# Optimization experiments

Hardware: AMD Instinct MI355X
Metric: run time of the kernel (lower is better)

## Reference

```python
import jax, jax.numpy as jnp
import numpy as np

N = 50000    # n_nodes
E = 800000   # n_edges (avg degree 16)
F_IN = 64    # node_features
F_H = 64     # filters


def setup_inputs() -> dict:
    key = jax.random.key(0)
    ks = jax.random.split(key, 24)
    p = lambda k, s: jax.random.normal(k, s, dtype=jnp.float32) * 0.05
    inp = {
        "x": jax.random.normal(ks[0], (N, F_IN), dtype=jnp.float32),
        "edge_index": jax.random.randint(ks[1], (2, E), 0, N, dtype=jnp.int32),
        "edge_weight": jax.random.uniform(ks[2], (E,), dtype=jnp.float32),
    }
    # 6 ChebConvs (K=2): conv_x_z, conv_h_z, conv_x_r, conv_h_r, conv_x_h, conv_h_h
    for i, nm in enumerate(["xz", "hz", "xr", "hr", "xh", "hh"]):
        fin = F_IN if nm[0] == "x" else F_H
        inp[f"W_{nm}0"] = p(ks[3 + 3 * i], (fin, F_H))
        inp[f"W_{nm}1"] = p(ks[4 + 3 * i], (fin, F_H))
        inp[f"b_{nm}"] = p(ks[5 + 3 * i], (F_H,))
    inp["W_lin"] = p(ks[21], (F_H, F_IN))
    inp["b_lin"] = p(ks[22], (F_IN,))
    return inp


def _forward(x, edge_weight, edge_index,
             W_xz0, W_xz1, b_xz, W_hz0, W_hz1, b_hz,
             W_xr0, W_xr1, b_xr, W_hr0, W_hr1, b_hr,
             W_xh0, W_xh1, b_xh, W_hh0, W_hh1, b_hh,
             W_lin, b_lin):
    row, col = edge_index[0], edge_index[1]
    # ChebConv K=2, sym normalization, lambda_max=2: L_hat = -D^{-1/2} A D^{-1/2}
    # (self-loops removed first, as in PyG ChebConv)
    w = jnp.where(row == col, 0.0, edge_weight)
    deg = jax.ops.segment_sum(w, row, num_segments=N)
    deg_safe = jnp.where(deg > 0, deg, 1.0)
    dinv = jnp.where(deg > 0, jax.lax.rsqrt(deg_safe), 0.0)
    norm = -dinv[row] * w * dinv[col]  # [E]

    def conv(v, W0, W1, b):
        # Tx_0 = v ; Tx_1 = L_hat @ v via gather-scatter along edges
        tx1 = jax.ops.segment_sum(norm[:, None] * v[row], col, num_segments=N)
        return v @ W0 + tx1 @ W1 + b

    H = jnp.zeros((N, F_H), dtype=x.dtype)  # initial hidden state
    Z = jax.nn.sigmoid(conv(x, W_xz0, W_xz1, b_xz) + conv(H, W_hz0, W_hz1, b_hz))
    R = jax.nn.sigmoid(conv(x, W_xr0, W_xr1, b_xr) + conv(H, W_hr0, W_hr1, b_hr))
    Ht = jnp.tanh(conv(x, W_xh0, W_xh1, b_xh) + conv(H * R, W_hh0, W_hh1, b_hh))
    H = Z * H + (1.0 - Z) * Ht
    return jax.nn.relu(H) @ W_lin + b_lin


def reference(x, edge_index, edge_weight,
              W_xz0, W_xz1, b_xz, W_hz0, W_hz1, b_hz,
              W_xr0, W_xr1, b_xr, W_hr0, W_hr1, b_hr,
              W_xh0, W_xh1, b_xh, W_hh0, W_hh1, b_hh,
              W_lin, b_lin):
    return _forward(x, edge_weight, edge_index,
                    W_xz0, W_xz1, b_xz, W_hz0, W_hz1, b_hz,
                    W_xr0, W_xr1, b_xr, W_hr0, W_hr1, b_hr,
                    W_xh0, W_xh1, b_xh, W_hh0, W_hh1, b_hh,
                    W_lin, b_lin)
```

## Files before the change

### kernel.cpp

```cpp
#include <hip/hip_runtime.h>

#define N_NODES 50000
#define N_EDGES 800000
#define F 64
#define NPAD 50048
#define NBUCK 196
#define NBLK 256
#define EPB (N_EDGES / NBLK)
#define BN 128
#define AIDX32(k, n) ((k) * 132 + ((k) >> 3) * 4 + (n))

typedef float f32x4 __attribute__((ext_vector_type(4)));
typedef short bf16x8 __attribute__((ext_vector_type(8)));

__device__ inline unsigned short f2bf(float f) {
    unsigned u = __float_as_uint(f);
    u = (u + 0x7FFFu + ((u >> 16) & 1u)) >> 16;
    return (unsigned short)u;
}

__global__ __launch_bounds__(256) void prep_w(const float* __restrict__ Wxz0,
                                              const float* __restrict__ Wxz1,
                                              const float* __restrict__ Wxh0,
                                              const float* __restrict__ Wxh1,
                                              const float* __restrict__ Wlin,
                                              unsigned short* __restrict__ wzT,
                                              unsigned short* __restrict__ whT,
                                              unsigned short* __restrict__ wlT) {
    int gid = blockIdx.x * 256 + threadIdx.x;
    int m = gid >> 12, idx = gid & 4095;
    int k = idx >> 6, f = idx & 63;
    const float* src;
    unsigned short* dst;
    if (m == 0)      { src = Wxz0; dst = wzT; }
    else if (m == 1) { src = Wxz1; dst = wzT + 4096; }
    else if (m == 2) { src = Wxh0; dst = whT; }
    else if (m == 3) { src = Wxh1; dst = whT + 4096; }
    else             { src = Wlin; dst = wlT; }
    dst[f * 64 + k] = f2bf(src[idx]);
}

__global__ __launch_bounds__(256) void prep_x(const float* __restrict__ x,
                                              unsigned short* __restrict__ xb) {
    int idx4 = blockIdx.x * 256 + threadIdx.x;
    int n = idx4 >> 4;
    ushort4 o = make_ushort4(0, 0, 0, 0);
    if (n < N_NODES) {
        float4 v = *(const float4*)&x[idx4 * 4];
        o = make_ushort4(f2bf(v.x), f2bf(v.y), f2bf(v.z), f2bf(v.w));
    }
    *(ushort4*)&xb[idx4 * 4] = o;
}

__global__ __launch_bounds__(256) void count_kernel(const int* __restrict__ ei,
                                                    int* __restrict__ cntC,
                                                    int* __restrict__ cntR) {
    __shared__ int histC[NBUCK], histR[NBUCK];
    const int t = threadIdx.x, blk = blockIdx.x;
    for (int i = t; i < NBUCK; i += 256) { histC[i] = 0; histR[i] = 0; }
    __syncthreads();
    const int e0 = blk * EPB;
    for (int i = t; i < EPB; i += 256) {
        int e = e0 + i;
        int r = ei[e], c = ei[N_EDGES + e];
        if (r != c) {
            atomicAdd(&histC[c >> 8], 1);
            atomicAdd(&histR[r >> 8], 1);
        }
    }
    __syncthreads();
    for (int i = t; i < NBUCK; i += 256) {
        cntC[i * NBLK + blk] = histC[i];
        cntR[i * NBLK + blk] = histR[i];
    }
}

__global__ __launch_bounds__(256) void scan1_kernel(int* __restrict__ cntC,
                                                    int* __restrict__ cntR,
                                                    int* __restrict__ btC,
                                                    int* __restrict__ btR) {
    __shared__ int wsum[4];
    const int t = threadIdx.x, g = blockIdx.x;
    int* cnt = (g < NBUCK) ? cntC : cntR;
    int* bt  = (g < NBUCK) ? btC : btR;
    const int bucket = (g < NBUCK) ? g : g - NBUCK;
    const int lane = t & 63, wid = t >> 6;
    int v = cnt[bucket * NBLK + t];
    int s = v;
#pragma unroll
    for (int d = 1; d < 64; d <<= 1) {
        int u = __shfl_up(s, d);
        if (lane >= d) s += u;
    }
    if (lane == 63) wsum[wid] = s;
    __syncthreads();
    int wbase = 0;
    for (int w = 0; w < wid; ++w) wbase += wsum[w];
    cnt[bucket * NBLK + t] = wbase + s - v;
    if (t == 255) bt[bucket] = wbase + s;
}

__global__ __launch_bounds__(256) void scan2_kernel(const int* __restrict__ btC,
                                                    const int* __restrict__ btR,
                                                    int* __restrict__ bbC,
                                                    int* __restrict__ bbR,
                                                    int* __restrict__ offs) {
    __shared__ int wsum[4];
    const int t = threadIdx.x;
    const int lane = t & 63, wid = t >> 6;
    {
        int v = (t < NBUCK) ? btC[t] : 0;
        int s = v;
#pragma unroll
        for (int d = 1; d < 64; d <<= 1) {
            int u = __shfl_up(s, d);
            if (lane >= d) s += u;
        }
        if (lane == 63) wsum[wid] = s;
        __syncthreads();
        int wbase = 0;
        for (int w = 0; w < wid; ++w) wbase += wsum[w];
        if (t < NBUCK) bbC[t] = wbase + s - v;
        if (t == 255) { bbC[NBUCK] = wbase + s; offs[N_NODES] = wbase + s; }
        __syncthreads();
    }
    {
        int v = (t < NBUCK) ? btR[t] : 0;
        int s = v;
#pragma unroll
        for (int d = 1; d < 64; d <<= 1) {
            int u = __shfl_up(s, d);
            if (lane >= d) s += u;
        }
        if (lane == 63) wsum[wid] = s;
        __syncthreads();
        int wbase = 0;
        for (int w = 0; w < wid; ++w) wbase += wsum[w];
        if (t < NBUCK) bbR[t] = wbase + s - v;
        if (t == 255) bbR[NBUCK] = wbase + s;
    }
}

__global__ __launch_bounds__(256) void place_kernel(const int* __restrict__ ei,
                                                    const float* __restrict__ ew,
                                                    const int* __restrict__ cntC,
                                                    const int* __restrict__ cntR,
                                                    const int* __restrict__ bbC,
                                                    const int* __restrict__ bbR,
                                                    uint2* __restrict__ colPart,
                                                    uint2* __restrict__ rowPart) {
    __shared__ int cursC[NBUCK], cursR[NBUCK];
    const int t = threadIdx.x, blk = blockIdx.x;
    for (int i = t; i < NBUCK; i += 256) {
        cursC[i] = bbC[i] + cntC[i * NBLK + blk];
        cursR[i] = bbR[i] + cntR[i * NBLK + blk];
    }
    __syncthreads();
    const int e0 = blk * EPB;
    for (int i = t; i < EPB; i += 256) {
        int e = e0 + i;
        int r = ei[e], c = ei[N_EDGES + e];
        if (r == c) continue;
        unsigned wbits = __float_as_uint(ew[e]);
        int pC = atomicAdd(&cursC[c >> 8], 1);
        colPart[pC] = make_uint2((unsigned)r | ((unsigned)(c & 255) << 16), wbits);
        int pR = atomicAdd(&cursR[r >> 8], 1);
        rowPart[pR] = make_uint2((unsigned)(r & 255), wbits);
    }
}

__global__ __launch_bounds__(256) void rowB_kernel(const uint2* __restrict__ rowPart,
                                                   const int* __restrict__ bbR,
                                                   float* __restrict__ dinv) {
    __shared__ float degL[256];
    const int t = threadIdx.x, b = blockIdx.x;
    degL[t] = 0.0f;
    __syncthreads();
    const int start = bbR[b], end = bbR[b + 1];
    for (int i = start + t; i < end; i += 256) {
        uint2 v = rowPart[i];
        atomicAdd(&degL[v.x], __uint_as_float(v.y));
    }
    __syncthreads();
    int n = b * 256 + t;
    if (n < N_NODES) {
        float d = degL[t];
        dinv[n] = (d > 0.0f) ? rsqrtf(d) : 0.0f;
    }
}

__global__ __launch_bounds__(256) void colB_kernel(const uint2* __restrict__ colPart,
                                                   const int* __restrict__ bbC,
                                                   const float* __restrict__ dinv,
                                                   int* __restrict__ offs,
                                                   uint2* __restrict__ edgesOut) {
    __shared__ int cntL[256];
    __shared__ int curL[256];
    __shared__ int wsum[4];
    const int t = threadIdx.x, b = blockIdx.x;
    const int lane = t & 63, wid = t >> 6;
    const int start = bbC[b], end = bbC[b + 1];
    cntL[t] = 0;
    __syncthreads();
    for (int i = start + t; i < end; i += 256) {
        uint2 v = colPart[i];
        atomicAdd(&cntL[(v.x >> 16) & 255], 1);
    }
    __syncthreads();
    int v = cntL[t];
    int s = v;
#pragma unroll
    for (int d = 1; d < 64; d <<= 1) {
        int u = __shfl_up(s, d);
        if (lane >= d) s += u;
    }
    if (lane == 63) wsum[wid] = s;
    __syncthreads();
    int wbase = 0;
    for (int w = 0; w < wid; ++w) wbase += wsum[w];
    int excl = wbase + s - v;
    curL[t] = excl;
    int n = b * 256 + t;
    if (n < N_NODES) offs[n] = start + excl;
    __syncthreads();
    for (int i = start + t; i < end; i += 256) {
        uint2 e = colPart[i];
        int cl = (e.x >> 16) & 255;
        int p = atomicAdd(&curL[cl], 1);
        int r = e.x & 0xFFFF;
        float wd = __uint_as_float(e.y) * dinv[r];
        edgesOut[start + p] = make_uint2((unsigned)r, __float_as_uint(wd));
    }
}

__global__ __launch_bounds__(256) void gather_kernel(const int* __restrict__ offs,
                                                     const uint2* __restrict__ edgesOut,
                                                     const float* __restrict__ dinv,
                                                     const float* __restrict__ x,
                                                     unsigned short* __restrict__ Sb) {
    int n = blockIdx.x * 4 + (threadIdx.x >> 6);
    int lane = threadIdx.x & 63;
    if (n >= N_NODES) return;
    int p = offs[n], end = offs[n + 1];
    float acc = 0.0f;
    for (int base = p; base < end; base += 32) {
        int rem = end - base;
        int sl = lane & 31;
        uint2 ev = make_uint2(0u, 0u);
        if (sl < rem) ev = edgesOut[base + sl];
        int myr = (int)ev.x;
        float mwd = __uint_as_float(ev.y);
        int cnt = min(rem, 32);
        int i = 0;
        for (; i + 4 <= cnt; i += 4) {
            int r0 = __shfl(myr, i + 0), r1 = __shfl(myr, i + 1);
            int r2 = __shfl(myr, i + 2), r3 = __shfl(myr, i + 3);
            float w0 = __shfl(mwd, i + 0), w1 = __shfl(mwd, i + 1);
            float w2 = __shfl(mwd, i + 2), w3 = __shfl(mwd, i + 3);
            float v0 = x[r0 * F + lane];
            float v1 = x[r1 * F + lane];
            float v2 = x[r2 * F + lane];
            float v3 = x[r3 * F + lane];
            acc = fmaf(w0, v0, acc);
            acc = fmaf(w1, v1, acc);
            acc = fmaf(w2, v2, acc);
            acc = fmaf(w3, v3, acc);
        }
        for (; i < cnt; ++i) {
            int r = __shfl(myr, i);
            float wd = __shfl(mwd, i);
            acc = fmaf(wd, x[r * F + lane], acc);
        }
    }
    Sb[n * F + lane] = f2bf(-dinv[n] * acc);
}

__global__ __launch_bounds__(256) void fused_mfma(
    const unsigned short* __restrict__ xb, const unsigned short* __restrict__ Sb,
    const unsigned short* __restrict__ wzT, const unsigned short* __restrict__ whT,
    const unsigned short* __restrict__ wlT,
    const float* __restrict__ bxz, const float* __restrict__ bhz,
    const float* __restrict__ bxh, const float* __restrict__ bhh,
    const float* __restrict__ blin, float* __restrict__ out) {
    __shared__ __align__(16) unsigned short Rlds[4 * 16 * 72];

    const int t = threadIdx.x;
    const int l = t & 63, wid = t >> 6;
    const int row16 = l & 15, quad = l >> 4;
    const int gn0 = blockIdx.x * 64 + wid * 16;

    f32x4 zacc[4], hacc[4];
#pragma unroll
    for (int ft = 0; ft < 4; ++ft) {
        int f = ft * 16 + row16;
        float bz = bxz[f] + bhz[f];
        float bh = bxh[f] + bhh[f];
        zacc[ft] = (f32x4){bz, bz, bz, bz};
        hacc[ft] = (f32x4){bh, bh, bh, bh};
    }

#pragma unroll
    for (int half = 0; half < 2; ++half) {
        const unsigned short* Ab = half ? Sb : xb;
        const unsigned short* Wzp = wzT + half * 4096;
        const unsigned short* Whp = whT + half * 4096;
#pragma unroll
        for (int ks = 0; ks < 2; ++ks) {
            bf16x8 a = *(const bf16x8*)(Ab + (size_t)(gn0 + row16) * 64 + ks * 32 + quad * 8);
#pragma unroll
            for (int ft = 0; ft < 4; ++ft) {
                bf16x8 bz8 = *(const bf16x8*)(Wzp + (ft * 16 + row16) * 64 + ks * 32 + quad * 8);
                bf16x8 bh8 = *(const bf16x8*)(Whp + (ft * 16 + row16) * 64 + ks * 32 + quad * 8);
                zacc[ft] = __builtin_amdgcn_mfma_f32_16x16x32_bf16(a, bz8, zacc[ft], 0, 0, 0);
                hacc[ft] = __builtin_amdgcn_mfma_f32_16x16x32_bf16(a, bh8, hacc[ft], 0, 0, 0);
            }
        }
    }

#pragma unroll
    for (int ft = 0; ft < 4; ++ft)
#pragma unroll
        for (int r = 0; r < 4; ++r) {
            float z = zacc[ft][r], h = hacc[ft][r];
            float zz = 1.0f / (1.0f + __expf(-z));
            float R = fmaxf((1.0f - zz) * tanhf(h), 0.0f);
            Rlds[wid * 1152 + (quad * 4 + r) * 72 + ft * 16 + row16] = f2bf(R);
        }

    f32x4 oacc[4];
#pragma unroll
    for (int ft = 0; ft < 4; ++ft) oacc[ft] = (f32x4){0.f, 0.f, 0.f, 0.f};
#pragma unroll
    for (int ks = 0; ks < 2; ++ks) {
        bf16x8 ra = *(const bf16x8*)&Rlds[wid * 1152 + row16 * 72 + ks * 32 + quad * 8];
#pragma unroll
        for (int ft = 0; ft < 4; ++ft) {
            bf16x8 wl8 = *(const bf16x8*)(wlT + (ft * 16 + row16) * 64 + ks * 32 + quad * 8);
            oacc[ft] = __builtin_amdgcn_mfma_f32_16x16x32_bf16(ra, wl8, oacc[ft], 0, 0, 0);
        }
    }
#pragma unroll
    for (int ft = 0; ft < 4; ++ft) {
        float bl = blin[ft * 16 + row16];
#pragma unroll
        for (int r = 0; r < 4; ++r) {
            int gn = gn0 + quad * 4 + r;
            if (gn < N_NODES) out[gn * 64 + ft * 16 + row16] = oacc[ft][r] + bl;
        }
    }
}

__global__ __launch_bounds__(256) void deg_fb(const int* __restrict__ ei,
                                              const float* __restrict__ ew,
                                              float* __restrict__ deg) {
    int e = blockIdx.x * blockDim.x + threadIdx.x;
    if (e >= N_EDGES) return;
    int r = ei[e];
    int c = ei[N_EDGES + e];
    if (r != c) atomicAdd(&deg[r], ew[e]);
}

__global__ __launch_bounds__(256) void dinv_kernel(const float* __restrict__ deg,
                                                   float* __restrict__ dinv) {
    int n = blockIdx.x * blockDim.x + threadIdx.x;
    if (n >= N_NODES) return;
    float d = deg[n];
    dinv[n] = (d > 0.0f) ? rsqrtf(d) : 0.0f;
}

__global__ __launch_bounds__(256) void scatter_fb(const int* __restrict__ ei,
                                                  const float* __restrict__ ew,
                                                  const float* __restrict__ x,
                                                  const float* __restrict__ dinv,
                                                  float* S) {
    int e = blockIdx.x * 4 + (threadIdx.x >> 6);
    int lane = threadIdx.x & 63;
    if (e >= N_EDGES) return;
    int r = ei[e];
    int c = ei[N_EDGES + e];
    if (r == c) return;
    float nrm = -dinv[r] * ew[e] * dinv[c];
    atomicAdd(&S[c * F + lane], nrm * x[r * F + lane]);
}

__global__ __launch_bounds__(128) void fused_fp32(
    const float* __restrict__ x, float* sOut,
    const float* __restrict__ Wxz0, const float* __restrict__ Wxz1,
    const float* __restrict__ Wxh0, const float* __restrict__ Wxh1,
    const float* __restrict__ bxz, const float* __restrict__ bhz,
    const float* __restrict__ bxh, const float* __restrict__ bhh,
    const float* __restrict__ Wlin, const float* __restrict__ blin) {
    __shared__ float P[8448];
    float* As = P;
    float* Wc = P + 4352;
    const int t = threadIdx.x;
    const int n0 = blockIdx.x * BN;
    const int ti = t >> 3;
    const int tj = t & 7;
    const int nb = ti * 8;
    const int f0 = tj * 8;

    float zacc[8][8], hacc[8][8];
#pragma unroll
    for (int j = 0; j < 8; ++j) {
        float bz = bxz[f0 + j] + bhz[f0 + j];
        float bh = bxh[f0 + j] + bhh[f0 + j];
#pragma unroll
        for (int i = 0; i < 8; ++i) { zacc[i][j] = bz; hacc[i][j] = bh; }
    }
    for (int half = 0; half < 2; ++half) {
        const float* Abase = half ? (const float*)sOut : x;
        const float* Wz = half ? Wxz1 : Wxz0;
        const float* Wh = half ? Wxh1 : Wxh0;
        for (int kc = 0; kc < 2; ++kc) {
            const int kb = kc * 32;
            __syncthreads();
#pragma unroll
            for (int rep = 0; rep < 8; ++rep) {
                int idx = rep * 128 + t;
                int nn = idx >> 3;
                int q = idx & 7;
                int gn = n0 + nn;
                float4 v = make_float4(0.f, 0.f, 0.f, 0.f);
                if (gn < N_NODES) v = *(const float4*)&Abase[gn * F + kb + q * 4];
                int k = q * 4;
                As[AIDX32(k + 0, nn)] = v.x;
                As[AIDX32(k + 1, nn)] = v.y;
                As[AIDX32(k + 2, nn)] = v.z;
                As[AIDX32(k + 3, nn)] = v.w;
            }
#pragma unroll
            for (int rep = 0; rep < 8; ++rep) {
                int idx = rep * 128 + t;
                int cq = idx & 31;
                int kk = idx >> 5;
                const float* src = (cq < 16) ? &Wz[(kb + kk) * F + cq * 4]
                                             : &Wh[(kb + kk) * F + (cq - 16) * 4];
                *(float4*)&Wc[kk * 128 + cq * 4] = *(const float4*)src;
            }
            __syncthreads();
#pragma unroll 8
            for (int kl = 0; kl < 32; ++kl) {
                const float* Ap = &As[AIDX32(kl, nb)];
                float4 a0 = *(const float4*)Ap;
                float4 a1 = *(const float4*)(Ap + 4);
                const float* Wp = &Wc[kl * 128 + f0];
                float4 wz0 = *(const float4*)Wp;
                float4 wz1 = *(const float4*)(Wp + 4);
                float4 wh0 = *(const float4*)(Wp + 64);
                float4 wh1 = *(const float4*)(Wp + 68);
                float a[8]  = {a0.x, a0.y, a0.z, a0.w, a1.x, a1.y, a1.z, a1.w};
                float wz[8] = {wz0.x, wz0.y, wz0.z, wz0.w, wz1.x, wz1.y, wz1.z, wz1.w};
                float wh[8] = {wh0.x, wh0.y, wh0.z, wh0.w, wh1.x, wh1.y, wh1.z, wh1.w};
#pragma unroll
                for (int i = 0; i < 8; ++i)
#pragma unroll
                    for (int j = 0; j < 8; ++j) {
                        zacc[i][j] = fmaf(a[i], wz[j], zacc[i][j]);
                        hacc[i][j] = fmaf(a[i], wh[j], hacc[i][j]);
                    }
            }
        }
    }
    __syncthreads();
#pragma unroll
    for (int j = 0; j < 8; ++j) {
        int f = f0 + j;
        float R[8];
#pragma unroll
        for (int i = 0; i < 8; ++i) {
            float zz = 1.0f / (1.0f + __expf(-zacc[i][j]));
            float hh = tanhf(hacc[i][j]);
            R[i] = fmaxf((1.0f - zz) * hh, 0.0f);
        }
        float* Rp = &P[f * 132 + nb];
        *(float4*)Rp = make_float4(R[0], R[1], R[2], R[3]);
        *(float4*)(Rp + 4) = make_float4(R[4], R[5], R[6], R[7]);
    }
    __syncthreads();
    float (*oacc)[8] = zacc;
#pragma unroll
    for (int j = 0; j < 8; ++j) {
        float bl = blin[f0 + j];
#pragma unroll
        for (int i = 0; i < 8; ++i) oacc[i][j] = bl;
    }
#pragma unroll 4
    for (int k = 0; k < 64; ++k) {
        const float* Rp = &P[k * 132 + nb];
        float4 a0 = *(const float4*)Rp;
        float4 a1 = *(const float4*)(Rp + 4);
        float4 w0 = *(const float4*)&Wlin[k * F + f0];
        float4 w1 = *(const float4*)&Wlin[k * F + f0 + 4];
        float a[8] = {a0.x, a0.y, a0.z, a0.w, a1.x, a1.y, a1.z, a1.w};
        float w[8] = {w0.x, w0.y, w0.z, w0.w, w1.x, w1.y, w1.z, w1.w};
#pragma unroll
        for (int i = 0; i < 8; ++i)
#pragma unroll
            for (int j = 0; j < 8; ++j)
                oacc[i][j] = fmaf(a[i], w[j], oacc[i][j]);
    }
#pragma unroll
    for (int i = 0; i < 8; ++i) {
        int gn = n0 + nb + i;
        if (gn < N_NODES) {
            *(float4*)&sOut[gn * F + f0] =
                make_float4(oacc[i][0], oacc[i][1], oacc[i][2], oacc[i][3]);
            *(float4*)&sOut[gn * F + f0 + 4] =
                make_float4(oacc[i][4], oacc[i][5], oacc[i][6], oacc[i][7]);
        }
    }
}

extern "C" void kernel_launch(void* const* d_in, const int* in_sizes, int n_in,
                              void* d_out, int out_size, void* d_ws, size_t ws_size,
                              hipStream_t stream) {
    const float* x    = (const float*)d_in[0];
    const int*   ei   = (const int*)d_in[1];
    const float* ew   = (const float*)d_in[2];
    const float* Wxz0 = (const float*)d_in[3];
    const float* Wxz1 = (const float*)d_in[4];
    const float* bxz  = (const float*)d_in[5];
    const float* bhz  = (const float*)d_in[8];
    const float* Wxh0 = (const float*)d_in[15];
    const float* Wxh1 = (const float*)d_in[16];
    const float* bxh  = (const float*)d_in[17];
    const float* bhh  = (const float*)d_in[20];
    const float* Wlin = (const float*)d_in[21];
    const float* blin = (const float*)d_in[22];
    float* outp = (float*)d_out;

    int*    cntC  = (int*)d_ws;
    int*    cntR  = cntC + NBUCK * NBLK;
    int*    btC   = cntR + NBUCK * NBLK;
    int*    btR   = btC + 256;
    int*    bbC   = btR + 256;
    int*    bbR   = bbC + 256;
    int*    offs  = bbR + 256;
    float*  dinv  = (float*)(offs + NPAD + 64);
    unsigned short* xb  = (unsigned short*)(dinv + NPAD);
    unsigned short* Sb  = xb + (size_t)NPAD * 64;
    unsigned short* wzT = Sb + (size_t)NPAD * 64;
    unsigned short* whT = wzT + 8192;
    unsigned short* wlT = whT + 8192;
    uint2*  colPart  = (uint2*)(wlT + 4096);
    uint2*  rowPart  = colPart + N_EDGES;
    uint2*  edgesOut = rowPart + N_EDGES;
    size_t needed = (size_t)(2 * NBUCK * NBLK + 1024 + NPAD + 64 + NPAD) * 4
                  + (size_t)NPAD * 64 * 2 * 2 + 40960
                  + (size_t)N_EDGES * 3 * 8 + 256;

    if (ws_size >= needed) {
        prep_w<<<80, 256, 0, stream>>>(Wxz0, Wxz1, Wxh0, Wxh1, Wlin, wzT, whT, wlT);
        prep_x<<<NPAD * 16 / 256, 256, 0, stream>>>(x, xb);
        count_kernel<<<NBLK, 256, 0, stream>>>(ei, cntC, cntR);
        scan1_kernel<<<2 * NBUCK, 256, 0, stream>>>(cntC, cntR, btC, btR);
        scan2_kernel<<<1, 256, 0, stream>>>(btC, btR, bbC, bbR, offs);
        place_kernel<<<NBLK, 256, 0, stream>>>(ei, ew, cntC, cntR, bbC, bbR,
                                               colPart, rowPart);
        rowB_kernel<<<NBUCK, 256, 0, stream>>>(rowPart, bbR, dinv);
        colB_kernel<<<NBUCK, 256, 0, stream>>>(colPart, bbC, dinv, offs, edgesOut);
        gather_kernel<<<(N_NODES + 3) / 4, 256, 0, stream>>>(offs, edgesOut, dinv,
                                                             x, Sb);
        fused_mfma<<<NPAD / 64, 256, 0, stream>>>(xb, Sb, wzT, whT, wlT,
                                                  bxz, bhz, bxh, bhh, blin, outp);
    } else {
        float* deg = (float*)d_ws;
        float* dv  = deg + NPAD;
        hipMemsetAsync(deg, 0, (size_t)NPAD * sizeof(float), stream);
        hipMemsetAsync(d_out, 0, (size_t)N_NODES * F * sizeof(float), stream);
        deg_fb<<<(N_EDGES + 255) / 256, 256, 0, stream>>>(ei, ew, deg);
        dinv_kernel<<<(N_NODES + 255) / 256, 256, 0, stream>>>(deg, dv);
        scatter_fb<<<N_EDGES / 4, 256, 0, stream>>>(ei, ew, x, dv, outp);
        fused_fp32<<<(N_NODES + BN - 1) / BN, 128, 0, stream>>>(
            x, outp, Wxz0, Wxz1, Wxh0, Wxh1, bxz, bhz, bxh, bhh, Wlin, blin);
    }
}
```

Baseline: 122.5 us.

## Replace CSR build plus gather with per-bucket LDS atomic accumulation

Column buckets shrink to 128 nodes, so each bucket's 128x64 fp32 partial sum fits in shared memory. A new 1024-thread kernel processes each bucket's edges directly, using shared-memory atomics instead of building a sorted per-node CSR (colB plus edgesOut) and running a separate gather pass. This removes one kernel launch and an 800k-edge intermediate write and read. The two prep kernels are also merged into one launch. The trade-off is LDS atomic contention, and fp32 summation order that is no longer deterministic.

```diff
diff --git a/kernel.cpp b/kernel.cpp
--- a/kernel.cpp
+++ b/kernel.cpp
@@ -4,7 +4,8 @@
 #define N_EDGES 800000
 #define F 64
 #define NPAD 50048
-#define NBUCK 196
+#define NBUCKC 392
+#define NBUCKR 196
 #define NBLK 256
 #define EPB (N_EDGES / NBLK)
 #define BN 128
@@ -19,60 +20,58 @@
     return (unsigned short)u;
 }
 
-__global__ __launch_bounds__(256) void prep_w(const float* __restrict__ Wxz0,
-                                              const float* __restrict__ Wxz1,
-                                              const float* __restrict__ Wxh0,
-                                              const float* __restrict__ Wxh1,
-                                              const float* __restrict__ Wlin,
-                                              unsigned short* __restrict__ wzT,
-                                              unsigned short* __restrict__ whT,
-                                              unsigned short* __restrict__ wlT) {
-    int gid = blockIdx.x * 256 + threadIdx.x;
-    int m = gid >> 12, idx = gid & 4095;
-    int k = idx >> 6, f = idx & 63;
-    const float* src;
-    unsigned short* dst;
-    if (m == 0)      { src = Wxz0; dst = wzT; }
-    else if (m == 1) { src = Wxz1; dst = wzT + 4096; }
-    else if (m == 2) { src = Wxh0; dst = whT; }
-    else if (m == 3) { src = Wxh1; dst = whT + 4096; }
-    else             { src = Wlin; dst = wlT; }
-    dst[f * 64 + k] = f2bf(src[idx]);
-}
-
-__global__ __launch_bounds__(256) void prep_x(const float* __restrict__ x,
-                                              unsigned short* __restrict__ xb) {
-    int idx4 = blockIdx.x * 256 + threadIdx.x;
-    int n = idx4 >> 4;
-    ushort4 o = make_ushort4(0, 0, 0, 0);
-    if (n < N_NODES) {
-        float4 v = *(const float4*)&x[idx4 * 4];
-        o = make_ushort4(f2bf(v.x), f2bf(v.y), f2bf(v.z), f2bf(v.w));
-    }
-    *(ushort4*)&xb[idx4 * 4] = o;
+__global__ __launch_bounds__(256) void prep_kernel(
+    const float* __restrict__ x,
+    const float* __restrict__ Wxz0, const float* __restrict__ Wxz1,
+    const float* __restrict__ Wxh0, const float* __restrict__ Wxh1,
+    const float* __restrict__ Wlin,
+    unsigned short* __restrict__ xb, unsigned short* __restrict__ wzT,
+    unsigned short* __restrict__ whT, unsigned short* __restrict__ wlT) {
+    int blk = blockIdx.x;
+    if (blk < 80) {
+        int gid = blk * 256 + threadIdx.x;
+        int m = gid >> 12, idx = gid & 4095;
+        int k = idx >> 6, f = idx & 63;
+        const float* src;
+        unsigned short* dst;
+        if (m == 0)      { src = Wxz0; dst = wzT; }
+        else if (m == 1) { src = Wxz1; dst = wzT + 4096; }
+        else if (m == 2) { src = Wxh0; dst = whT; }
+        else if (m == 3) { src = Wxh1; dst = whT + 4096; }
+        else             { src = Wlin; dst = wlT; }
+        dst[f * 64 + k] = f2bf(src[idx]);
+    } else {
+        int idx4 = (blk - 80) * 256 + threadIdx.x;
+        int n = idx4 >> 4;
+        ushort4 o = make_ushort4(0, 0, 0, 0);
+        if (n < N_NODES) {
+            float4 v = *(const float4*)&x[idx4 * 4];
+            o = make_ushort4(f2bf(v.x), f2bf(v.y), f2bf(v.z), f2bf(v.w));
+        }
+        *(ushort4*)&xb[idx4 * 4] = o;
+    }
 }
 
 __global__ __launch_bounds__(256) void count_kernel(const int* __restrict__ ei,
                                                     int* __restrict__ cntC,
                                                     int* __restrict__ cntR) {
-    __shared__ int histC[NBUCK], histR[NBUCK];
+    __shared__ int histC[NBUCKC], histR[NBUCKR];
     const int t = threadIdx.x, blk = blockIdx.x;
-    for (int i = t; i < NBUCK; i += 256) { histC[i] = 0; histR[i] = 0; }
+    for (int i = t; i < NBUCKC; i += 256) histC[i] = 0;
+    for (int i = t; i < NBUCKR; i += 256) histR[i] = 0;
     __syncthreads();
     const int e0 = blk * EPB;
     for (int i = t; i < EPB; i += 256) {
         int e = e0 + i;
         int r = ei[e], c = ei[N_EDGES + e];
         if (r != c) {
-            atomicAdd(&histC[c >> 8], 1);
+            atomicAdd(&histC[c >> 7], 1);
             atomicAdd(&histR[r >> 8], 1);
         }
     }
     __syncthreads();
-    for (int i = t; i < NBUCK; i += 256) {
-        cntC[i * NBLK + blk] = histC[i];
-        cntR[i * NBLK + blk] = histR[i];
-    }
+    for (int i = t; i < NBUCKC; i += 256) cntC[i * NBLK + blk] = histC[i];
+    for (int i = t; i < NBUCKR; i += 256) cntR[i * NBLK + blk] = histR[i];
 }
 
 __global__ __launch_bounds__(256) void scan1_kernel(int* __restrict__ cntC,
@@ -81,9 +80,9 @@
                                                     int* __restrict__ btR) {
     __shared__ int wsum[4];
     const int t = threadIdx.x, g = blockIdx.x;
-    int* cnt = (g < NBUCK) ? cntC : cntR;
-    int* bt  = (g < NBUCK) ? btC : btR;
-    const int bucket = (g < NBUCK) ? g : g - NBUCK;
+    int* cnt; int* bt; int bucket;
+    if (g < NBUCKC) { cnt = cntC; bt = btC; bucket = g; }
+    else            { cnt = cntR; bt = btR; bucket = g - NBUCKC; }
     const int lane = t & 63, wid = t >> 6;
     int v = cnt[bucket * NBLK + t];
     int s = v;
@@ -103,13 +102,14 @@
 __global__ __launch_bounds__(256) void scan2_kernel(const int* __restrict__ btC,
                                                     const int* __restrict__ btR,
                                                     int* __restrict__ bbC,
-                                                    int* __restrict__ bbR,
-                                                    int* __restrict__ offs) {
+                                                    int* __restrict__ bbR) {
     __shared__ int wsum[4];
     const int t = threadIdx.x;
     const int lane = t & 63, wid = t >> 6;
-    {
-        int v = (t < NBUCK) ? btC[t] : 0;
+    int total = 0;
+    for (int chunk = 0; chunk < 2; ++chunk) {
+        int i = chunk * 256 + t;
+        int v = (i < NBUCKC) ? btC[i] : 0;
         int s = v;
 #pragma unroll
         for (int d = 1; d < 64; d <<= 1) {
@@ -120,12 +120,14 @@
         __syncthreads();
         int wbase = 0;
         for (int w = 0; w < wid; ++w) wbase += wsum[w];
-        if (t < NBUCK) bbC[t] = wbase + s - v;
-        if (t == 255) { bbC[NBUCK] = wbase + s; offs[N_NODES] = wbase + s; }
+        if (i < NBUCKC) bbC[i] = total + wbase + s - v;
+        int btot = wsum[0] + wsum[1] + wsum[2] + wsum[3];
         __syncthreads();
-    }
+        total += btot;
+    }
+    if (t == 0) bbC[NBUCKC] = total;
     {
-        int v = (t < NBUCK) ? btR[t] : 0;
+        int v = (t < NBUCKR) ? btR[t] : 0;
         int s = v;
 #pragma unroll
         for (int d = 1; d < 64; d <<= 1) {
@@ -136,8 +138,8 @@
         __syncthreads();
         int wbase = 0;
         for (int w = 0; w < wid; ++w) wbase += wsum[w];
-        if (t < NBUCK) bbR[t] = wbase + s - v;
-        if (t == 255) bbR[NBUCK] = wbase + s;
+        if (t < NBUCKR) bbR[t] = wbase + s - v;
+        if (t == 255) bbR[NBUCKR] = wbase + s;
     }
 }
 
@@ -149,12 +151,10 @@
                                                     const int* __restrict__ bbR,
                                                     uint2* __restrict__ colPart,
                                                     uint2* __restrict__ rowPart) {
-    __shared__ int cursC[NBUCK], cursR[NBUCK];
+    __shared__ int cursC[NBUCKC], cursR[NBUCKR];
     const int t = threadIdx.x, blk = blockIdx.x;
-    for (int i = t; i < NBUCK; i += 256) {
-        cursC[i] = bbC[i] + cntC[i * NBLK + blk];
-        cursR[i] = bbR[i] + cntR[i * NBLK + blk];
-    }
+    for (int i = t; i < NBUCKC; i += 256) cursC[i] = bbC[i] + cntC[i * NBLK + blk];
+    for (int i = t; i < NBUCKR; i += 256) cursR[i] = bbR[i] + cntR[i * NBLK + blk];
     __syncthreads();
     const int e0 = blk * EPB;
     for (int i = t; i < EPB; i += 256) {
@@ -162,8 +162,8 @@
         int r = ei[e], c = ei[N_EDGES + e];
         if (r == c) continue;
         unsigned wbits = __float_as_uint(ew[e]);
-        int pC = atomicAdd(&cursC[c >> 8], 1);
-        colPart[pC] = make_uint2((unsigned)r | ((unsigned)(c & 255) << 16), wbits);
+        int pC = atomicAdd(&cursC[c >> 7], 1);
+        colPart[pC] = make_uint2((unsigned)r | ((unsigned)(c & 127) << 16), wbits);
         int pR = atomicAdd(&cursR[r >> 8], 1);
         rowPart[pR] = make_uint2((unsigned)(r & 255), wbits);
     }
@@ -189,90 +189,46 @@
     }
 }
 
-__global__ __launch_bounds__(256) void colB_kernel(const uint2* __restrict__ colPart,
-                                                   const int* __restrict__ bbC,
-                                                   const float* __restrict__ dinv,
-                                                   int* __restrict__ offs,
-                                                   uint2* __restrict__ edgesOut) {
-    __shared__ int cntL[256];
-    __shared__ int curL[256];
-    __shared__ int wsum[4];
+__global__ __launch_bounds__(1024) void gatherB_kernel(const uint2* __restrict__ colPart,
+                                                       const int* __restrict__ bbC,
+                                                       const float* __restrict__ dinv,
+                                                       const float* __restrict__ x,
+                                                       unsigned short* __restrict__ Sb) {
+    __shared__ float Sl[128 * 64];
     const int t = threadIdx.x, b = blockIdx.x;
-    const int lane = t & 63, wid = t >> 6;
+    const int lane = t & 63, wv = t >> 6;
+#pragma unroll
+    for (int rep = 0; rep < 8; ++rep) Sl[rep * 1024 + t] = 0.0f;
+    __syncthreads();
     const int start = bbC[b], end = bbC[b + 1];
-    cntL[t] = 0;
-    __syncthreads();
-    for (int i = start + t; i < end; i += 256) {
-        uint2 v = colPart[i];
-        atomicAdd(&cntL[(v.x >> 16) & 255], 1);
-    }
-    __syncthreads();
-    int v = cntL[t];
-    int s = v;
-#pragma unroll
-    for (int d = 1; d < 64; d <<= 1) {
-        int u = __shfl_up(s, d);
-        if (lane >= d) s += u;
-    }
-    if (lane == 63) wsum[wid] = s;
-    __syncthreads();
-    int wbase = 0;
-    for (int w = 0; w < wid; ++w) wbase += wsum[w];
-    int excl = wbase + s - v;
-    curL[t] = excl;
-    int n = b * 256 + t;
-    if (n < N_NODES) offs[n] = start + excl;
-    __syncthreads();
-    for (int i = start + t; i < end; i += 256) {
-        uint2 e = colPart[i];
-        int cl = (e.x >> 16) & 255;
-        int p = atomicAdd(&curL[cl], 1);
-        int r = e.x & 0xFFFF;
-        float wd = __uint_as_float(e.y) * dinv[r];
-        edgesOut[start + p] = make_uint2((unsigned)r, __float_as_uint(wd));
-    }
-}
-
-__global__ __launch_bounds__(256) void gather_kernel(const int* __restrict__ offs,
-                                                     const uint2* __restrict__ edgesOut,
-                                                     const float* __restrict__ dinv,
-                                                     const float* __restrict__ x,
-                                                     unsigned short* __restrict__ Sb) {
-    int n = blockIdx.x * 4 + (threadIdx.x >> 6);
-    int lane = threadIdx.x & 63;
-    if (n >= N_NODES) return;
-    int p = offs[n], end = offs[n + 1];
-    float acc = 0.0f;
-    for (int base = p; base < end; base += 32) {
-        int rem = end - base;
-        int sl = lane & 31;
-        uint2 ev = make_uint2(0u, 0u);
-        if (sl < rem) ev = edgesOut[base + sl];
-        int myr = (int)ev.x;
-        float mwd = __uint_as_float(ev.y);
-        int cnt = min(rem, 32);
-        int i = 0;
-        for (; i + 4 <= cnt; i += 4) {
-            int r0 = __shfl(myr, i + 0), r1 = __shfl(myr, i + 1);
-            int r2 = __shfl(myr, i + 2), r3 = __shfl(myr, i + 3);
-            float w0 = __shfl(mwd, i + 0), w1 = __shfl(mwd, i + 1);
-            float w2 = __shfl(mwd, i + 2), w3 = __shfl(mwd, i + 3);
-            float v0 = x[r0 * F + lane];
-            float v1 = x[r1 * F + lane];
-            float v2 = x[r2 * F + lane];
-            float v3 = x[r3 * F + lane];
-            acc = fmaf(w0, v0, acc);
-            acc = fmaf(w1, v1, acc);
-            acc = fmaf(w2, v2, acc);
-            acc = fmaf(w3, v3, acc);
-        }
-        for (; i < cnt; ++i) {
-            int r = __shfl(myr, i);
-            float wd = __shfl(mwd, i);
-            acc = fmaf(wd, x[r * F + lane], acc);
-        }
-    }
-    Sb[n * F + lane] = f2bf(-dinv[n] * acc);
+    int i = start + wv;
+    for (; i + 16 < end; i += 32) {
+        uint2 e0 = colPart[i];
+        uint2 e1 = colPart[i + 16];
+        int r0 = e0.x & 0xFFFF, r1 = e1.x & 0xFFFF;
+        int c0 = (e0.x >> 16) & 127, c1 = (e1.x >> 16) & 127;
+        float w0 = __uint_as_float(e0.y) * dinv[r0];
+        float w1 = __uint_as_float(e1.y) * dinv[r1];
+        float x0 = x[r0 * F + lane];
+        float x1 = x[r1 * F + lane];
+        atomicAdd(&Sl[c0 * 64 + lane], w0 * x0);
+        atomicAdd(&Sl[c1 * 64 + lane], w1 * x1);
+    }
+    if (i < end) {
+        uint2 e0 = colPart[i];
+        int r0 = e0.x & 0xFFFF;
+        int c0 = (e0.x >> 16) & 127;
+        float w0 = __uint_as_float(e0.y) * dinv[r0];
+        atomicAdd(&Sl[c0 * 64 + lane], w0 * x[r0 * F + lane]);
+    }
+    __syncthreads();
+    const int n0 = b * 128;
+#pragma unroll
+    for (int rep = 0; rep < 8; ++rep) {
+        int idx = rep * 1024 + t;
+        int n = n0 + (idx >> 6);
+        if (n < N_NODES) Sb[(size_t)n * F + (idx & 63)] = f2bf(-dinv[n] * Sl[idx]);
+    }
 }
 
 __global__ __launch_bounds__(256) void fused_mfma(
@@ -531,37 +487,33 @@
     float* outp = (float*)d_out;
 
     int*    cntC  = (int*)d_ws;
-    int*    cntR  = cntC + NBUCK * NBLK;
-    int*    btC   = cntR + NBUCK * NBLK;
-    int*    btR   = btC + 256;
+    int*    cntR  = cntC + NBUCKC * NBLK;
+    int*    btC   = cntR + NBUCKR * NBLK;
+    int*    btR   = btC + 512;
     int*    bbC   = btR + 256;
-    int*    bbR   = bbC + 256;
-    int*    offs  = bbR + 256;
-    float*  dinv  = (float*)(offs + NPAD + 64);
+    int*    bbR   = bbC + 512;
+    float*  dinv  = (float*)(bbR + 256);
     unsigned short* xb  = (unsigned short*)(dinv + NPAD);
     unsigned short* Sb  = xb + (size_t)NPAD * 64;
     unsigned short* wzT = Sb + (size_t)NPAD * 64;
     unsigned short* whT = wzT + 8192;
     unsigned short* wlT = whT + 8192;
-    uint2*  colPart  = (uint2*)(wlT + 4096);
-    uint2*  rowPart  = colPart + N_EDGES;
-    uint2*  edgesOut = rowPart + N_EDGES;
-    size_t needed = (size_t)(2 * NBUCK * NBLK + 1024 + NPAD + 64 + NPAD) * 4
+    uint2*  colPart = (uint2*)(wlT + 4096);
+    uint2*  rowPart = colPart + N_EDGES;
+    size_t needed = (size_t)(NBUCKC * NBLK + NBUCKR * NBLK + 1536 + NPAD) * 4
                   + (size_t)NPAD * 64 * 2 * 2 + 40960
-                  + (size_t)N_EDGES * 3 * 8 + 256;
+                  + (size_t)N_EDGES * 2 * 8 + 256;
 
     if (ws_size >= needed) {
-        prep_w<<<80, 256, 0, stream>>>(Wxz0, Wxz1, Wxh0, Wxh1, Wlin, wzT, whT, wlT);
-        prep_x<<<NPAD * 16 / 256, 256, 0, stream>>>(x, xb);
+        prep_kernel<<<80 + NPAD * 16 / 256, 256, 0, stream>>>(
+            x, Wxz0, Wxz1, Wxh0, Wxh1, Wlin, xb, wzT, whT, wlT);
         count_kernel<<<NBLK, 256, 0, stream>>>(ei, cntC, cntR);
-        scan1_kernel<<<2 * NBUCK, 256, 0, stream>>>(cntC, cntR, btC, btR);
-        scan2_kernel<<<1, 256, 0, stream>>>(btC, btR, bbC, bbR, offs);
+        scan1_kernel<<<NBUCKC + NBUCKR, 256, 0, stream>>>(cntC, cntR, btC, btR);
+        scan2_kernel<<<1, 256, 0, stream>>>(btC, btR, bbC, bbR);
         place_kernel<<<NBLK, 256, 0, stream>>>(ei, ew, cntC, cntR, bbC, bbR,
                                                colPart, rowPart);
-        rowB_kernel<<<NBUCK, 256, 0, stream>>>(rowPart, bbR, dinv);
-        colB_kernel<<<NBUCK, 256, 0, stream>>>(colPart, bbC, dinv, offs, edgesOut);
-        gather_kernel<<<(N_NODES + 3) / 4, 256, 0, stream>>>(offs, edgesOut, dinv,
-                                                             x, Sb);
+        rowB_kernel<<<NBUCKR, 256, 0, stream>>>(rowPart, bbR, dinv);
+        gatherB_kernel<<<NBUCKC, 1024, 0, stream>>>(colPart, bbC, dinv, x, Sb);
         fused_mfma<<<NPAD / 64, 256, 0, stream>>>(xb, Sb, wzT, whT, wlT,
                                                   bxz, bhz, bxh, bhh, blin, outp);
     } else {
```

Result: slower. 424.2 us (+246.3%).
